# Performance work log

Hardware: AMD Instinct MI355X
Metric: run time of the kernel (lower is better)

## Reference

```python
import jax, jax.numpy as jnp
import numpy as np

# B=batch, T=time, H=hidden_size, D=vocos_dim, I=intermediate_dim, L=num_layers,
# CB=codebook_size, CD=codebook_dim (factorized VQ)
B, T, H, D, I, L, CB, CD = 8, 2048, 1024, 384, 2048, 12, 8192, 8


def _ln(h, g, b, eps=1e-6):
    # torch LayerNorm over last dim (biased variance)
    m = h.mean(-1, keepdims=True)
    v = h.var(-1, keepdims=True)
    return (h - m) / jnp.sqrt(v + eps) * g + b


def _conv1d(x, w, b, groups=1):
    # x: (B, Cin, T), w: (Cout, Cin//groups, 7), same-pad k=7
    y = jax.lax.conv_general_dilated(
        x, w, window_strides=(1,), padding=[(3, 3)],
        dimension_numbers=('NCH', 'OIH', 'NCH'), feature_group_count=groups)
    return y + b[None, :, None]


def setup_inputs() -> dict:
    key = jax.random.key(0)
    ks = iter(jax.random.split(key, 32))
    def nrm(shape):
        return jax.random.normal(next(ks), shape, jnp.float32) * 0.02
    d = {}
    d['x'] = jax.random.normal(next(ks), (B, T, H), jnp.float32)
    # VocosBackbone (encoder): embed conv + LN + 12 ConvNeXt blocks + final LN
    d['enc_embed_w'] = nrm((D, H, 7)); d['enc_embed_b'] = jnp.zeros((D,), jnp.float32)
    d['enc_norm_g'] = jnp.ones((D,), jnp.float32); d['enc_norm_b'] = jnp.zeros((D,), jnp.float32)
    d['enc_dw_w'] = nrm((L, D, 1, 7)); d['enc_dw_b'] = jnp.zeros((L, D), jnp.float32)
    d['enc_ln_g'] = jnp.ones((L, D), jnp.float32); d['enc_ln_b'] = jnp.zeros((L, D), jnp.float32)
    d['enc_w1'] = nrm((L, I, D)); d['enc_b1'] = jnp.zeros((L, I), jnp.float32)
    d['enc_w2'] = nrm((L, D, I)); d['enc_b2'] = jnp.zeros((L, D), jnp.float32)
    d['enc_gamma'] = jnp.full((L, D), 1.0 / L, jnp.float32)  # layer_scale init 1/num_layers
    d['enc_fnorm_g'] = jnp.ones((D,), jnp.float32); d['enc_fnorm_b'] = jnp.zeros((D,), jnp.float32)
    # nn.Linear(vocos_dim, hidden_size)
    d['enc_out_w'] = nrm((H, D)); d['enc_out_b'] = jnp.zeros((H,), jnp.float32)
    # Factorized ResidualVQ (single quantizer): 1024 -> 8, 8192-entry codebook, 8 -> 1024
    d['vq_in_w'] = nrm((CD, H)); d['vq_in_b'] = jnp.zeros((CD,), jnp.float32)
    d['codebook'] = jax.random.normal(next(ks), (CB, CD), jnp.float32)
    d['vq_out_w'] = nrm((H, CD)); d['vq_out_b'] = jnp.zeros((H,), jnp.float32)
    return d


def _encode(x, ew, eb, ng, nb, dww, dwb, lng, lnb, w1, b1, w2, b2, gamma, fg, fb, ow, ob):
    # x: (B, T, H) -> encoder output (B, T, H)
    h = _conv1d(x.transpose(0, 2, 1), ew, eb)            # (B, D, T)
    h = _ln(h.transpose(0, 2, 1), ng, nb)                # (B, T, D)
    for i in range(L):
        res = h
        y = _conv1d(h.transpose(0, 2, 1), dww[i], dwb[i], groups=D)  # depthwise (B, D, T)
        y = _ln(y.transpose(0, 2, 1), lng[i], lnb[i])                # (B, T, D)
        y = jax.nn.gelu(y @ w1[i].T + b1[i], approximate=False)       # (B, T, I)
        y = (y @ w2[i].T + b2[i]) * gamma[i]                          # (B, T, D)
        h = res + y
    h = _ln(h, fg, fb)
    return h @ ow.T + ob                                  # (B, T, H)


def _quantize(enc, in_w, in_b, codebook, out_w, out_b):
    z_e = enc @ in_w.T + in_b                             # (B, T, CD)
    z_n = z_e / jnp.maximum(jnp.linalg.norm(z_e, axis=-1, keepdims=True), 1e-12)
    cb_n = codebook / jnp.maximum(jnp.linalg.norm(codebook, axis=-1, keepdims=True), 1e-12)
    sim = jnp.einsum('btd,nd->btn', z_n, cb_n)            # cosine sim == argmin l2 on normalized vecs
    idx = jnp.argmax(sim, axis=-1)                        # (B, T) int
    z_q = codebook[idx]                                   # (B, T, CD) unnormalized codebook entries
    z_q = z_e + jax.lax.stop_gradient(z_q - z_e)          # straight-through estimator
    quantized = z_q @ out_w.T + out_b                     # (B, T, H)
    return idx, quantized


def reference(x, enc_embed_w, enc_embed_b, enc_norm_g, enc_norm_b, enc_dw_w, enc_dw_b,
              enc_ln_g, enc_ln_b, enc_w1, enc_b1, enc_w2, enc_b2, enc_gamma,
              enc_fnorm_g, enc_fnorm_b, enc_out_w, enc_out_b,
              vq_in_w, vq_in_b, codebook, vq_out_w, vq_out_b):
    enc = _encode(x, enc_embed_w, enc_embed_b, enc_norm_g, enc_norm_b, enc_dw_w, enc_dw_b,
                  enc_ln_g, enc_ln_b, enc_w1, enc_b1, enc_w2, enc_b2, enc_gamma,
                  enc_fnorm_g, enc_fnorm_b, enc_out_w, enc_out_b)
    idx, quantized = _quantize(enc, vq_in_w, vq_in_b, codebook, vq_out_w, vq_out_b)
    # RepCodec.quantize returns (indices (B,T), quantized_out.transpose(1,2) -> (B,T,H))
    return idx, quantized
```

## Files before the change

### kernel.cpp

```cpp
#include <hip/hip_runtime.h>
#include <math.h>


typedef _Float16 h8_t __attribute__((ext_vector_type(8)));
typedef _Float16 h4_t __attribute__((ext_vector_type(4)));
typedef float f4_t __attribute__((ext_vector_type(4)));

__device__ __forceinline__ float gelu_exact(float x){
  return 0.5f * x * (1.0f + erff(x * 0.70710678118654752f));
}

__device__ __forceinline__ void split4(const float4& a, h4_t& hi, h4_t& lo){
  float f[4] = {a.x,a.y,a.z,a.w};
  #pragma unroll
  for (int t=0;t<4;t++){
    _Float16 hh = (_Float16)f[t];
    hi[t] = hh;
    lo[t] = (_Float16)(f[t] - (float)hh);
  }
}

__device__ __forceinline__ int swz(int row, int kg){
  return row*32 + ((kg ^ ((row>>1)&3))<<3);
}

__device__ __forceinline__ void xcd_remap(int& bx, int& by){
  const int gx = gridDim.x;
  const int nwg = gx * gridDim.y;
  int bid = by*gx + bx;
  if ((nwg & 7) == 0){
    bid = (bid & 7)*(nwg >> 3) + (bid >> 3);
    bx = bid % gx; by = bid / gx;
  }
}


__global__ __launch_bounds__(256) void prep_wk_split(const float* __restrict__ w,
                                                     _Float16* __restrict__ wh,
                                                     _Float16* __restrict__ wl){
  int i = blockIdx.x*256 + threadIdx.x;
  if (i >= 384*1024) return;
  int d = i >> 10, c = i & 1023;
  #pragma unroll
  for (int k=0;k<7;k++){
    float v = w[(size_t)d*(1024*7) + (size_t)c*7 + k];
    _Float16 hh = (_Float16)v;
    wh[(size_t)k*393216 + i] = hh;
    wl[(size_t)k*393216 + i] = (_Float16)(v - (float)hh);
  }
}

__global__ __launch_bounds__(256) void prep_cb(const float* __restrict__ cb, float* __restrict__ cbn){
  int e = blockIdx.x*256 + threadIdx.x;
  if (e >= 8192) return;
  float v[8], s = 0.f;
  #pragma unroll
  for (int cd=0; cd<8; ++cd){ v[cd] = cb[(size_t)e*8+cd]; s += v[cd]*v[cd]; }
  float inv = 1.0f / fmaxf(sqrtf(s), 1e-12f);
  #pragma unroll
  for (int cd=0; cd<8; ++cd) cbn[(size_t)e*8+cd] = v[cd]*inv;
}

__global__ __launch_bounds__(256) void split_pair(const float* __restrict__ a, const float* __restrict__ b,
                                                  _Float16* __restrict__ ah, _Float16* __restrict__ al,
                                                  _Float16* __restrict__ bh, _Float16* __restrict__ bl,
                                                  int n4){
  int i = blockIdx.x*256 + threadIdx.x;
  if (i >= n4) return;
  h4_t hi, lo;
  float4 va = ((const float4*)a)[i];
  split4(va, hi, lo);
  ((h4_t*)ah)[i] = hi; ((h4_t*)al)[i] = lo;
  float4 vb = ((const float4*)b)[i];
  split4(vb, hi, lo);
  ((h4_t*)bh)[i] = hi; ((h4_t*)bl)[i] = lo;
}

__global__ __launch_bounds__(256) void split_one(const float* __restrict__ a,
                                                 _Float16* __restrict__ ah, _Float16* __restrict__ al,
                                                 int n4){
  int i = blockIdx.x*256 + threadIdx.x;
  if (i >= n4) return;
  h4_t hi, lo;
  float4 va = ((const float4*)a)[i];
  split4(va, hi, lo);
  ((h4_t*)ah)[i] = hi; ((h4_t*)al)[i] = lo;
}

template<int BN, int EPI>
__global__ __launch_bounds__(256,2) void gemm_s(
    const _Float16* __restrict__ Ah, const _Float16* __restrict__ Al, int lda,
    const _Float16* __restrict__ Bh, const _Float16* __restrict__ Bl, int ldb,
    const float* __restrict__ bias, const float* __restrict__ gamma,
    float* __restrict__ C, _Float16* __restrict__ Ch, _Float16* __restrict__ Cl,
    int ldc, int K)
{
  constexpr int NF = BN/32;
  __shared__ _Float16 AsH[4096], AsL[4096];
  __shared__ _Float16 BsH[BN*32], BsL[BN*32];
  const int tid = threadIdx.x;
  int bx = blockIdx.x, by = blockIdx.y;
  xcd_remap(bx, by);
  const int m0 = by*128, n0 = bx*BN;
  const int srow = tid>>2, kgs = tid&3, koff = kgs*8;
  const _Float16* pAh = Ah + (size_t)(m0+srow)*lda + koff;
  const _Float16* pAl = Al + (size_t)(m0+srow)*lda + koff;
  const _Float16* pBh = Bh + (size_t)(n0+srow)*ldb + koff;
  const _Float16* pBl = Bl + (size_t)(n0+srow)*ldb + koff;
  const int sA0 = swz(srow, kgs), sA1 = swz(srow+64, kgs);
  const int lane = tid & 63, wid = tid >> 6;
  const int wm = (wid>>1)*64, wn = (wid&1)*(BN/2);
  const int fr = lane & 15, kg = lane >> 4;
  f4_t acc[4][NF] = {};
  h8_t rah0 = *(const h8_t*)(pAh);
  h8_t rah1 = *(const h8_t*)(pAh + (size_t)64*lda);
  h8_t ral0 = *(const h8_t*)(pAl);
  h8_t ral1 = *(const h8_t*)(pAl + (size_t)64*lda);
  h8_t rbh0 = *(const h8_t*)(pBh);
  h8_t rbl0 = *(const h8_t*)(pBl);
  h8_t rbh1, rbl1;
  if constexpr (BN == 128){
    rbh1 = *(const h8_t*)(pBh + (size_t)64*ldb);
    rbl1 = *(const h8_t*)(pBl + (size_t)64*ldb);
  }
  for (int k0 = 0; k0 < K; k0 += 32){
    __syncthreads();
    *(h8_t*)(AsH + sA0) = rah0; *(h8_t*)(AsL + sA0) = ral0;
    *(h8_t*)(AsH + sA1) = rah1; *(h8_t*)(AsL + sA1) = ral1;
    *(h8_t*)(BsH + sA0) = rbh0; *(h8_t*)(BsL + sA0) = rbl0;
    if constexpr (BN == 128){
      *(h8_t*)(BsH + sA1) = rbh1; *(h8_t*)(BsL + sA1) = rbl1;
    }
    if (k0 + 32 < K){
      const int kn = k0 + 32;
      rah0 = *(const h8_t*)(pAh + kn);
      rah1 = *(const h8_t*)(pAh + (size_t)64*lda + kn);
      ral0 = *(const h8_t*)(pAl + kn);
      ral1 = *(const h8_t*)(pAl + (size_t)64*lda + kn);
      rbh0 = *(const h8_t*)(pBh + kn);
      rbl0 = *(const h8_t*)(pBl + kn);
      if constexpr (BN == 128){
        rbh1 = *(const h8_t*)(pBh + (size_t)64*ldb + kn);
        rbl1 = *(const h8_t*)(pBl + (size_t)64*ldb + kn);
      }
    }
    __syncthreads();
    h8_t ah[4], al[4], bh[NF], bl[NF];
    #pragma unroll
    for (int m=0;m<4;m++){
      int o = swz(wm + fr + m*16, kg);
      ah[m] = *(const h8_t*)(AsH + o);
      al[m] = *(const h8_t*)(AsL + o);
    }
    #pragma unroll
    for (int n=0;n<NF;n++){
      int o = swz(wn + fr + n*16, kg);
      bh[n] = *(const h8_t*)(BsH + o);
      bl[n] = *(const h8_t*)(BsL + o);
    }
    #pragma unroll
    for (int m=0;m<4;m++)
      #pragma unroll
      for (int n=0;n<NF;n++){
        acc[m][n] = __builtin_amdgcn_mfma_f32_16x16x32_f16(al[m], bh[n], acc[m][n], 0,0,0);
        acc[m][n] = __builtin_amdgcn_mfma_f32_16x16x32_f16(ah[m], bl[n], acc[m][n], 0,0,0);
        acc[m][n] = __builtin_amdgcn_mfma_f32_16x16x32_f16(ah[m], bh[n], acc[m][n], 0,0,0);
      }
  }
  float bj[NF], gj[NF];
  #pragma unroll
  for (int n=0;n<NF;n++){
    int col = n0 + wn + n*16 + fr;
    bj[n] = bias ? bias[col] : 0.0f;
    gj[n] = (EPI==2) ? gamma[col] : 0.0f;
  }
  #pragma unroll
  for (int m=0;m<4;m++){
    #pragma unroll
    for (int r=0;r<4;r++){
      const int row = m0 + wm + m*16 + kg*4 + r;
      #pragma unroll
      for (int n=0;n<NF;n++){
        const int col = n0 + wn + n*16 + fr;
        float v = acc[m][n][r] + bj[n];
        if (EPI==0){
          C[(size_t)row*ldc + col] = v;
        } else if (EPI==1){
          v = gelu_exact(v);
          _Float16 hh = (_Float16)v;
          Ch[(size_t)row*ldc + col] = hh;
          Cl[(size_t)row*ldc + col] = (_Float16)(v - (float)hh);
        } else if (EPI==2){
          C[(size_t)row*ldc + col] += gj[n]*v;
        } else {
          _Float16 hh = (_Float16)v;
          Ch[(size_t)row*ldc + col] = hh;
          Cl[(size_t)row*ldc + col] = (_Float16)(v - (float)hh);
        }
      }
    }
  }
}

template<int EPI>
__global__ __launch_bounds__(512,2) void gemm_t(
    const _Float16* __restrict__ Ah, const _Float16* __restrict__ Al, int lda,
    const _Float16* __restrict__ Bh, const _Float16* __restrict__ Bl, int ldb,
    const float* __restrict__ bias,
    _Float16* __restrict__ Ch, _Float16* __restrict__ Cl,
    int ldc, int K)
{
  __shared__ _Float16 AsH[8192], AsL[8192], BsH[4096], BsL[4096];
  const int tid = threadIdx.x;
  int bx = blockIdx.x, by = blockIdx.y;
  xcd_remap(bx, by);
  const int m0 = by*256, n0 = bx*128;
  const int srow = tid>>2, kgs = tid&3, koff = kgs*8;
  const _Float16* pAh = Ah + (size_t)(m0+srow)*lda + koff;
  const _Float16* pAl = Al + (size_t)(m0+srow)*lda + koff;
  const _Float16* pBh = Bh + (size_t)(n0+srow)*ldb + koff;
  const _Float16* pBl = Bl + (size_t)(n0+srow)*ldb + koff;
  const int sA0 = swz(srow, kgs), sA1 = swz(srow+128, kgs);
  const int lane = tid & 63, wid = tid >> 6;
  const int wm = (wid>>1)*64, wn = (wid&1)*64;
  const int fr = lane & 15, kg = lane >> 4;
  f4_t acc[4][4] = {};
  h8_t rah0 = *(const h8_t*)(pAh);
  h8_t rah1 = *(const h8_t*)(pAh + (size_t)128*lda);
  h8_t ral0 = *(const h8_t*)(pAl);
  h8_t ral1 = *(const h8_t*)(pAl + (size_t)128*lda);
  h8_t rbh0 = *(const h8_t*)(pBh);
  h8_t rbl0 = *(const h8_t*)(pBl);
  for (int k0 = 0; k0 < K; k0 += 32){
    __syncthreads();
    *(h8_t*)(AsH + sA0) = rah0; *(h8_t*)(AsL + sA0) = ral0;
    *(h8_t*)(AsH + sA1) = rah1; *(h8_t*)(AsL + sA1) = ral1;
    *(h8_t*)(BsH + sA0) = rbh0; *(h8_t*)(BsL + sA0) = rbl0;
    if (k0 + 32 < K){
      const int kn = k0 + 32;
      rah0 = *(const h8_t*)(pAh + kn);
      rah1 = *(const h8_t*)(pAh + (size_t)128*lda + kn);
      ral0 = *(const h8_t*)(pAl + kn);
      ral1 = *(const h8_t*)(pAl + (size_t)128*lda + kn);
      rbh0 = *(const h8_t*)(pBh + kn);
      rbl0 = *(const h8_t*)(pBl + kn);
    }
    __syncthreads();
    h8_t ah[4], al[4], bh[4], bl[4];
    #pragma unroll
    for (int m=0;m<4;m++){
      int o = swz(wm + fr + m*16, kg);
      ah[m] = *(const h8_t*)(AsH + o);
      al[m] = *(const h8_t*)(AsL + o);
    }
    #pragma unroll
    for (int n=0;n<4;n++){
      int o = swz(wn + fr + n*16, kg);
      bh[n] = *(const h8_t*)(BsH + o);
      bl[n] = *(const h8_t*)(BsL + o);
    }
    #pragma unroll
    for (int m=0;m<4;m++)
      #pragma unroll
      for (int n=0;n<4;n++){
        acc[m][n] = __builtin_amdgcn_mfma_f32_16x16x32_f16(al[m], bh[n], acc[m][n], 0,0,0);
        acc[m][n] = __builtin_amdgcn_mfma_f32_16x16x32_f16(ah[m], bl[n], acc[m][n], 0,0,0);
        acc[m][n] = __builtin_amdgcn_mfma_f32_16x16x32_f16(ah[m], bh[n], acc[m][n], 0,0,0);
      }
  }
  float bj[4];
  #pragma unroll
  for (int n=0;n<4;n++){
    int col = n0 + wn + n*16 + fr;
    bj[n] = bias ? bias[col] : 0.0f;
  }
  #pragma unroll
  for (int m=0;m<4;m++){
    #pragma unroll
    for (int r=0;r<4;r++){
      const int row = m0 + wm + m*16 + kg*4 + r;
      #pragma unroll
      for (int n=0;n<4;n++){
        const int col = n0 + wn + n*16 + fr;
        float v = acc[m][n][r] + bj[n];
        if (EPI==1) v = gelu_exact(v);
        _Float16 hh = (_Float16)v;
        Ch[(size_t)row*ldc + col] = hh;
        Cl[(size_t)row*ldc + col] = (_Float16)(v - (float)hh);
      }
    }
  }
}

__global__ __launch_bounds__(256,2) void embed_f16(
    const _Float16* __restrict__ xh, const _Float16* __restrict__ xl,
    const _Float16* __restrict__ wkh, const _Float16* __restrict__ wkl,
    const float* __restrict__ bias, float* __restrict__ C)
{
  __shared__ _Float16 AsH[4096], AsL[4096], BsH[2048], BsL[2048];
  const int tid = threadIdx.x;
  int bx = blockIdx.x, by = blockIdx.y;
  xcd_remap(bx, by);
  const int m0 = by*128, n0 = bx*64;
  const int srow = tid>>2, kgs = tid&3, koff = kgs*8;
  const int sA0 = swz(srow, kgs), sA1 = swz(srow+64, kgs);
  const int lane = tid & 63, wid = tid >> 6;
  const int wm = (wid>>1)*64, wn = (wid&1)*32;
  const int fr = lane & 15, kg = lane >> 4;
  const int r0 = m0 + srow, r1 = r0 + 64;
  const int t0 = r0 & 2047, t1 = r1 & 2047;
  f4_t acc[4][2] = {};
  const h8_t zero8 = {0,0,0,0,0,0,0,0};
  h8_t rah0, rah1, ral0, ral1, rbh0, rbl0;
  auto load_tile = [&](int kt, h8_t& a0, h8_t& a1, h8_t& l0, h8_t& l1, h8_t& bh, h8_t& bl){
    const int k = kt >> 5;
    const int k0 = (kt & 31) << 5;
    const bool v0 = (unsigned)(t0 + k - 3) < 2048u;
    const bool v1 = (unsigned)(t1 + k - 3) < 2048u;
    a0 = zero8; a1 = zero8; l0 = zero8; l1 = zero8;
    if (v0){
      const size_t o = (size_t)(r0 + k - 3)*1024 + k0 + koff;
      a0 = *(const h8_t*)(xh + o); l0 = *(const h8_t*)(xl + o);
    }
    if (v1){
      const size_t o = (size_t)(r1 + k - 3)*1024 + k0 + koff;
      a1 = *(const h8_t*)(xh + o); l1 = *(const h8_t*)(xl + o);
    }
    const size_t wo = (size_t)k*393216 + (size_t)(n0+srow)*1024 + k0 + koff;
    bh = *(const h8_t*)(wkh + wo); bl = *(const h8_t*)(wkl + wo);
  };
  load_tile(0, rah0, rah1, ral0, ral1, rbh0, rbl0);
  for (int kt = 0; kt < 224; ++kt){
    __syncthreads();
    *(h8_t*)(AsH+sA0) = rah0; *(h8_t*)(AsL+sA0) = ral0;
    *(h8_t*)(AsH+sA1) = rah1; *(h8_t*)(AsL+sA1) = ral1;
    *(h8_t*)(BsH+sA0) = rbh0; *(h8_t*)(BsL+sA0) = rbl0;
    if (kt + 1 < 224)
      load_tile(kt+1, rah0, rah1, ral0, ral1, rbh0, rbl0);
    __syncthreads();
    h8_t ah[4], al[4], bh[2], bl[2];
    #pragma unroll
    for (int m=0;m<4;m++){
      int o = swz(wm + fr + m*16, kg);
      ah[m] = *(const h8_t*)(AsH + o);
      al[m] = *(const h8_t*)(AsL + o);
    }
    #pragma unroll
    for (int n=0;n<2;n++){
      int o = swz(wn + fr + n*16, kg);
      bh[n] = *(const h8_t*)(BsH + o);
      bl[n] = *(const h8_t*)(BsL + o);
    }
    #pragma unroll
    for (int m=0;m<4;m++)
      #pragma unroll
      for (int n=0;n<2;n++){
        acc[m][n] = __builtin_amdgcn_mfma_f32_16x16x32_f16(al[m], bh[n], acc[m][n], 0,0,0);
        acc[m][n] = __builtin_amdgcn_mfma_f32_16x16x32_f16(ah[m], bl[n], acc[m][n], 0,0,0);
        acc[m][n] = __builtin_amdgcn_mfma_f32_16x16x32_f16(ah[m], bh[n], acc[m][n], 0,0,0);
      }
  }
  #pragma unroll
  for (int m=0;m<4;m++){
    #pragma unroll
    for (int r=0;r<4;r++){
      const int row = m0 + wm + m*16 + kg*4 + r;
      #pragma unroll
      for (int n=0;n<2;n++){
        const int col = n0 + wn + n*16 + fr;
        C[(size_t)row*384 + col] = acc[m][n][r] + bias[col];
      }
    }
  }
}

template<bool CONV, bool SPLIT>
__global__ __launch_bounds__(384) void ln_kernel(
    const float* __restrict__ in,
    const float* __restrict__ dw, const float* __restrict__ db,
    const float* __restrict__ g, const float* __restrict__ b,
    float* __restrict__ out, _Float16* __restrict__ oh, _Float16* __restrict__ ol)
{
  __shared__ float rs[6], rs2[6], stat[2];
  const int m = blockIdx.x, d = threadIdx.x;
  float v;
  if (CONV){
    const int t = m & 2047;
    float a = db[d];
    #pragma unroll
    for (int k=0;k<7;k++){
      int tt = t + k - 3;
      if ((unsigned)tt < 2048u) a = fmaf(in[(size_t)(m + k - 3)*384 + d], dw[d*7 + k], a);
    }
    v = a;
  } else {
    v = in[(size_t)m*384 + d];
  }
  float s = v, s2 = v*v;
  #pragma unroll
  for (int o=1;o<64;o<<=1){ s += __shfl_xor(s,o); s2 += __shfl_xor(s2,o); }
  const int wid = d >> 6, lane = d & 63;
  if (lane == 0){ rs[wid]=s; rs2[wid]=s2; }
  __syncthreads();
  if (d == 0){
    float S=0.f, S2=0.f;
    #pragma unroll
    for (int w=0;w<6;w++){ S+=rs[w]; S2+=rs2[w]; }
    float mean = S*(1.0f/384.0f);
    float var = fmaxf(S2*(1.0f/384.0f) - mean*mean, 0.0f);
    stat[0]=mean; stat[1]=1.0f/sqrtf(var + 1e-6f);
  }
  __syncthreads();
  float o = (v - stat[0])*stat[1]*g[d] + b[d];
  if (SPLIT){
    _Float16 hh = (_Float16)o;
    oh[(size_t)m*384 + d] = hh;
    ol[(size_t)m*384 + d] = (_Float16)(o - (float)hh);
  } else {
    out[(size_t)m*384 + d] = o;
  }
}


__global__ __launch_bounds__(256) void vq_in_kernel(
    const _Float16* __restrict__ ench, const _Float16* __restrict__ encl,
    const float* __restrict__ wi, const float* __restrict__ bi, float* __restrict__ zn)
{
  __shared__ float sw[8192];
  const int tid = threadIdx.x;
  for (int i = tid*4; i < 8192; i += 1024) *(float4*)&sw[i] = *(const float4*)&wi[i];
  __syncthreads();
  const int wid = tid >> 6, lane = tid & 63;
  const size_t m = (size_t)blockIdx.x*4 + wid;
  float acc[8] = {};
  for (int j=0;j<16;j++){
    float v = (float)ench[m*1024 + j*64 + lane] + (float)encl[m*1024 + j*64 + lane];
    #pragma unroll
    for (int cd=0;cd<8;cd++) acc[cd] = fmaf(v, sw[cd*1024 + j*64 + lane], acc[cd]);
  }
  #pragma unroll
  for (int cd=0;cd<8;cd++)
    #pragma unroll
    for (int o=1;o<64;o<<=1) acc[cd] += __shfl_xor(acc[cd], o);
  if (lane == 0){
    float z[8], s = 0.f;
    #pragma unroll
    for (int cd=0;cd<8;cd++){ z[cd] = acc[cd] + bi[cd]; s += z[cd]*z[cd]; }
    float inv = 1.0f / fmaxf(sqrtf(s), 1e-12f);
    #pragma unroll
    for (int cd=0;cd<8;cd++) zn[m*8+cd] = z[cd]*inv;
  }
}

__global__ __launch_bounds__(256) void vq_argmax(
    const float* __restrict__ zn, const float* __restrict__ cbn,
    int* __restrict__ idx_out, float* __restrict__ idx_f)
{
  __shared__ float sbest[256];
  __shared__ int   sidx[256];
  const int tid = threadIdx.x;
  const int tok = tid & 31, ch = tid >> 5;
  const size_t m = (size_t)blockIdx.x*32 + tok;
  float4 z0 = *(const float4*)&zn[m*8];
  float4 z1 = *(const float4*)&zn[m*8+4];
  float best = -1e30f; int bidx = 0;
  const float* cp = cbn + (size_t)ch*8192;
  #pragma unroll 4
  for (int e = 0; e < 1024; ++e){
    const float4 ca  = *(const float4*)&cp[e*8];
    const float4 cb4 = *(const float4*)&cp[e*8+4];
    float s = z0.x*ca.x + z0.y*ca.y + z0.z*ca.z + z0.w*ca.w
            + z1.x*cb4.x + z1.y*cb4.y + z1.z*cb4.z + z1.w*cb4.w;
    if (s > best){ best = s; bidx = ch*1024 + e; }
  }
  sbest[tid] = best; sidx[tid] = bidx;
  __syncthreads();
  if (tid < 32){
    float b = sbest[tid]; int bi = sidx[tid];
    #pragma unroll
    for (int c=1;c<8;c++){
      float ob = sbest[c*32 + tid];
      if (ob > b){ b = ob; bi = sidx[c*32 + tid]; }
    }
    idx_out[(size_t)blockIdx.x*32 + tid] = bi;
    idx_f [(size_t)blockIdx.x*32 + tid] = (float)bi;
  }
}

__global__ __launch_bounds__(256) void vq_out_kernel(
    const int* __restrict__ idx, const float* __restrict__ cb,
    const float* __restrict__ wo, const float* __restrict__ bo,
    float* __restrict__ outq)
{
  __shared__ float wT[8][1024];
  __shared__ float cbs[16][8];
  __shared__ int idxs[16];
  const int tid = threadIdx.x;
  #pragma unroll
  for (int j=0;j<4;j++){
    int hcol = j*256 + tid;
    float4 w0 = *(const float4*)&wo[(size_t)hcol*8];
    float4 w1 = *(const float4*)&wo[(size_t)hcol*8+4];
    wT[0][hcol]=w0.x; wT[1][hcol]=w0.y; wT[2][hcol]=w0.z; wT[3][hcol]=w0.w;
    wT[4][hcol]=w1.x; wT[5][hcol]=w1.y; wT[6][hcol]=w1.z; wT[7][hcol]=w1.w;
  }
  if (tid < 16) idxs[tid] = idx[blockIdx.x*16 + tid];
  __syncthreads();
  if (tid < 128){ int tk = tid>>3, cd = tid&7; cbs[tk][cd] = cb[(size_t)idxs[tk]*8 + cd]; }
  __syncthreads();
  float bb[4];
  #pragma unroll
  for (int j=0;j<4;j++) bb[j] = bo[j*256+tid];
  for (int tk=0;tk<16;tk++){
    const size_t m = (size_t)blockIdx.x*16 + tk;
    float c0=cbs[tk][0], c1=cbs[tk][1], c2=cbs[tk][2], c3=cbs[tk][3];
    float c4=cbs[tk][4], c5=cbs[tk][5], c6=cbs[tk][6], c7=cbs[tk][7];
    #pragma unroll
    for (int j=0;j<4;j++){
      int hcol = j*256 + tid;
      float v = bb[j];
      v = fmaf(c0, wT[0][hcol], v); v = fmaf(c1, wT[1][hcol], v);
      v = fmaf(c2, wT[2][hcol], v); v = fmaf(c3, wT[3][hcol], v);
      v = fmaf(c4, wT[4][hcol], v); v = fmaf(c5, wT[5][hcol], v);
      v = fmaf(c6, wT[6][hcol], v); v = fmaf(c7, wT[7][hcol], v);
      outq[m*1024 + hcol] = v;
    }
  }
}


extern "C" void kernel_launch(void* const* d_in, const int* in_sizes, int n_in,
                              void* d_out, int out_size, void* d_ws, size_t ws_size,
                              hipStream_t stream) {
  (void)in_sizes; (void)n_in; (void)out_size; (void)ws_size;
  const float* x   = (const float*)d_in[0];
  const float* eww = (const float*)d_in[1];
  const float* ewb = (const float*)d_in[2];
  const float* ng  = (const float*)d_in[3];
  const float* nb  = (const float*)d_in[4];
  const float* dww = (const float*)d_in[5];
  const float* dwb = (const float*)d_in[6];
  const float* lng = (const float*)d_in[7];
  const float* lnb = (const float*)d_in[8];
  const float* w1  = (const float*)d_in[9];
  const float* b1  = (const float*)d_in[10];
  const float* w2  = (const float*)d_in[11];
  const float* b2  = (const float*)d_in[12];
  const float* gma = (const float*)d_in[13];
  const float* fg  = (const float*)d_in[14];
  const float* fb  = (const float*)d_in[15];
  const float* ow  = (const float*)d_in[16];
  const float* ob  = (const float*)d_in[17];
  const float* viw = (const float*)d_in[18];
  const float* vib = (const float*)d_in[19];
  const float* cb  = (const float*)d_in[20];
  const float* vow = (const float*)d_in[21];
  const float* vob = (const float*)d_in[22];
  float* out = (float*)d_out;

  float* ws = (float*)d_ws;
  float* wreg = ws;
  _Float16* wkh = (_Float16*)wreg;
  _Float16* wkl = wkh + 2752512;
  _Float16* w1h = (_Float16*)wreg;
  _Float16* w1l = w1h + 786432;
  _Float16* w2h = w1h + 1572864;
  _Float16* w2l = w1h + 2359296;
  _Float16* owh = (_Float16*)wreg;
  _Float16* owl = owh + 393216;
  float* zn  = wreg + 1048576;
  float* cbn = wreg + 1179648;
  int*  idxb = (int*)(wreg + 1245184);
  float* h   = ws + 2752512;
  float* ylreg = ws + 9043968;
  float* yf32 = ylreg;
  _Float16* ylh = (_Float16*)ylreg;
  _Float16* yll = ylh + 6291456;
  float* y1reg = ws + 15335424;
  _Float16* xh  = (_Float16*)y1reg;
  _Float16* xl  = xh + 16777216;
  _Float16* y1h = (_Float16*)y1reg;
  _Float16* y1l = y1h + 16777216;
  _Float16* ench = y1h;
  _Float16* encl = y1l;

  prep_wk_split<<<dim3(1536), dim3(256), 0, stream>>>(eww, wkh, wkl);
  split_one<<<dim3(16384), dim3(256), 0, stream>>>(x, xh, xl, 4194304);
  embed_f16<<<dim3(6,128), dim3(256), 0, stream>>>(xh, xl, wkh, wkl, ewb, yf32);
  ln_kernel<false,false><<<dim3(16384), dim3(384), 0, stream>>>(
      yf32, nullptr, nullptr, ng, nb, h, nullptr, nullptr);

  for (int i = 0; i < 12; ++i){
    split_pair<<<dim3(768), dim3(256), 0, stream>>>(
        w1 + (size_t)i*786432, w2 + (size_t)i*786432, w1h, w1l, w2h, w2l, 196608);
    ln_kernel<true,true><<<dim3(16384), dim3(384), 0, stream>>>(
        h, dww + (size_t)i*2688, dwb + (size_t)i*384,
        lng + (size_t)i*384, lnb + (size_t)i*384, nullptr, ylh, yll);
    for (int ic = 0; ic < 2; ++ic){
      gemm_t<1><<<dim3(8,64), dim3(512), 0, stream>>>(
          ylh, yll, 384,
          w1h + (size_t)ic*393216, w1l + (size_t)ic*393216, 384,
          b1 + (size_t)i*2048 + (size_t)ic*1024,
          y1h, y1l, 1024, 384);
      gemm_s<64,2><<<dim3(6,128), dim3(256), 0, stream>>>(
          y1h, y1l, 1024,
          w2h + (size_t)ic*1024, w2l + (size_t)ic*1024, 2048,
          (ic == 0) ? (b2 + (size_t)i*384) : nullptr,
          gma + (size_t)i*384,
          h, nullptr, nullptr, 384, 1024);
    }
  }

  ln_kernel<false,true><<<dim3(16384), dim3(384), 0, stream>>>(
      h, nullptr, nullptr, fg, fb, nullptr, ylh, yll);
  split_one<<<dim3(384), dim3(256), 0, stream>>>(ow, owh, owl, 98304);
  gemm_t<3><<<dim3(8,64), dim3(512), 0, stream>>>(
      ylh, yll, 384, owh, owl, 384, ob, ench, encl, 1024, 384);

  prep_cb<<<dim3(32), dim3(256), 0, stream>>>(cb, cbn);
  vq_in_kernel<<<dim3(4096), dim3(256), 0, stream>>>(ench, encl, viw, vib, zn);
  vq_argmax<<<dim3(512), dim3(256), 0, stream>>>(zn, cbn, idxb, out);
  vq_out_kernel<<<dim3(1024), dim3(256), 0, stream>>>(idxb, cb, vow, vob, out + 16384);
}
```

Measured before the change: 3.732 ms.

## Fold enc_out and vq_in projections, retile GEMMs with K=64 stages and setprio

Precomputes vq_in_w @ enc_out_w (8x384) and the matching combined bias, so the 1024-wide encoder output GEMM and its fp16 split are dropped and z_e is computed straight from the final LayerNorm output. The first FFN GEMM moves from gemm_t (256x128 tiles, 512 threads) to gemm_s<128> with 256 threads. The second FFN GEMM and the embed conv become a new gemm64-style kernel that stages 64-wide K tiles. MFMA blocks are wrapped in s_setprio. Folding the two linear maps changes the float rounding order, which could flip argmax ties, and the larger LDS tiles may lower occupancy.

```diff
diff --git a/kernel.cpp b/kernel.cpp
--- a/kernel.cpp
+++ b/kernel.cpp
@@ -59,6 +59,25 @@
   float inv = 1.0f / fmaxf(sqrtf(s), 1e-12f);
   #pragma unroll
   for (int cd=0; cd<8; ++cd) cbn[(size_t)e*8+cd] = v[cd]*inv;
+}
+
+__global__ __launch_bounds__(256) void prep_cw(const float* __restrict__ viw, const float* __restrict__ ow,
+                                               const float* __restrict__ vib, const float* __restrict__ ob,
+                                               float* __restrict__ cw, float* __restrict__ cbias){
+  int i = blockIdx.x*256 + threadIdx.x;
+  if (i < 3072){
+    int c = i / 384, d = i - c*384;
+    float acc = 0.f;
+    for (int h=0; h<1024; ++h)
+      acc = fmaf(viw[c*1024+h], ow[(size_t)h*384 + d], acc);
+    cw[i] = acc;
+  }
+  if (blockIdx.x == 0 && threadIdx.x < 8){
+    int c = threadIdx.x;
+    float acc = vib[c];
+    for (int h=0; h<1024; ++h) acc = fmaf(viw[c*1024+h], ob[h], acc);
+    cbias[c] = acc;
+  }
 }
 
 __global__ __launch_bounds__(256) void split_pair(const float* __restrict__ a, const float* __restrict__ b,
@@ -91,8 +110,8 @@
 __global__ __launch_bounds__(256,2) void gemm_s(
     const _Float16* __restrict__ Ah, const _Float16* __restrict__ Al, int lda,
     const _Float16* __restrict__ Bh, const _Float16* __restrict__ Bl, int ldb,
-    const float* __restrict__ bias, const float* __restrict__ gamma,
-    float* __restrict__ C, _Float16* __restrict__ Ch, _Float16* __restrict__ Cl,
+    const float* __restrict__ bias,
+    _Float16* __restrict__ Ch, _Float16* __restrict__ Cl,
     int ldc, int K)
 {
   constexpr int NF = BN/32;
@@ -158,6 +177,7 @@
       bh[n] = *(const h8_t*)(BsH + o);
       bl[n] = *(const h8_t*)(BsL + o);
     }
+    __builtin_amdgcn_s_setprio(1);
     #pragma unroll
     for (int m=0;m<4;m++)
       #pragma unroll
@@ -166,14 +186,11 @@
         acc[m][n] = __builtin_amdgcn_mfma_f32_16x16x32_f16(ah[m], bl[n], acc[m][n], 0,0,0);
         acc[m][n] = __builtin_amdgcn_mfma_f32_16x16x32_f16(ah[m], bh[n], acc[m][n], 0,0,0);
       }
-  }
-  float bj[NF], gj[NF];
-  #pragma unroll
-  for (int n=0;n<NF;n++){
-    int col = n0 + wn + n*16 + fr;
-    bj[n] = bias ? bias[col] : 0.0f;
-    gj[n] = (EPI==2) ? gamma[col] : 0.0f;
-  }
+    __builtin_amdgcn_s_setprio(0);
+  }
+  float bj[NF];
+  #pragma unroll
+  for (int n=0;n<NF;n++) bj[n] = bias ? bias[n0 + wn + n*16 + fr] : 0.0f;
   #pragma unroll
   for (int m=0;m<4;m++){
     #pragma unroll
@@ -181,106 +198,6 @@
       const int row = m0 + wm + m*16 + kg*4 + r;
       #pragma unroll
       for (int n=0;n<NF;n++){
-        const int col = n0 + wn + n*16 + fr;
-        float v = acc[m][n][r] + bj[n];
-        if (EPI==0){
-          C[(size_t)row*ldc + col] = v;
-        } else if (EPI==1){
-          v = gelu_exact(v);
-          _Float16 hh = (_Float16)v;
-          Ch[(size_t)row*ldc + col] = hh;
-          Cl[(size_t)row*ldc + col] = (_Float16)(v - (float)hh);
-        } else if (EPI==2){
-          C[(size_t)row*ldc + col] += gj[n]*v;
-        } else {
-          _Float16 hh = (_Float16)v;
-          Ch[(size_t)row*ldc + col] = hh;
-          Cl[(size_t)row*ldc + col] = (_Float16)(v - (float)hh);
-        }
-      }
-    }
-  }
-}
-
-template<int EPI>
-__global__ __launch_bounds__(512,2) void gemm_t(
-    const _Float16* __restrict__ Ah, const _Float16* __restrict__ Al, int lda,
-    const _Float16* __restrict__ Bh, const _Float16* __restrict__ Bl, int ldb,
-    const float* __restrict__ bias,
-    _Float16* __restrict__ Ch, _Float16* __restrict__ Cl,
-    int ldc, int K)
-{
-  __shared__ _Float16 AsH[8192], AsL[8192], BsH[4096], BsL[4096];
-  const int tid = threadIdx.x;
-  int bx = blockIdx.x, by = blockIdx.y;
-  xcd_remap(bx, by);
-  const int m0 = by*256, n0 = bx*128;
-  const int srow = tid>>2, kgs = tid&3, koff = kgs*8;
-  const _Float16* pAh = Ah + (size_t)(m0+srow)*lda + koff;
-  const _Float16* pAl = Al + (size_t)(m0+srow)*lda + koff;
-  const _Float16* pBh = Bh + (size_t)(n0+srow)*ldb + koff;
-  const _Float16* pBl = Bl + (size_t)(n0+srow)*ldb + koff;
-  const int sA0 = swz(srow, kgs), sA1 = swz(srow+128, kgs);
-  const int lane = tid & 63, wid = tid >> 6;
-  const int wm = (wid>>1)*64, wn = (wid&1)*64;
-  const int fr = lane & 15, kg = lane >> 4;
-  f4_t acc[4][4] = {};
-  h8_t rah0 = *(const h8_t*)(pAh);
-  h8_t rah1 = *(const h8_t*)(pAh + (size_t)128*lda);
-  h8_t ral0 = *(const h8_t*)(pAl);
-  h8_t ral1 = *(const h8_t*)(pAl + (size_t)128*lda);
-  h8_t rbh0 = *(const h8_t*)(pBh);
-  h8_t rbl0 = *(const h8_t*)(pBl);
-  for (int k0 = 0; k0 < K; k0 += 32){
-    __syncthreads();
-    *(h8_t*)(AsH + sA0) = rah0; *(h8_t*)(AsL + sA0) = ral0;
-    *(h8_t*)(AsH + sA1) = rah1; *(h8_t*)(AsL + sA1) = ral1;
-    *(h8_t*)(BsH + sA0) = rbh0; *(h8_t*)(BsL + sA0) = rbl0;
-    if (k0 + 32 < K){
-      const int kn = k0 + 32;
-      rah0 = *(const h8_t*)(pAh + kn);
-      rah1 = *(const h8_t*)(pAh + (size_t)128*lda + kn);
-      ral0 = *(const h8_t*)(pAl + kn);
-      ral1 = *(const h8_t*)(pAl + (size_t)128*lda + kn);
-      rbh0 = *(const h8_t*)(pBh + kn);
-      rbl0 = *(const h8_t*)(pBl + kn);
-    }
-    __syncthreads();
-    h8_t ah[4], al[4], bh[4], bl[4];
-    #pragma unroll
-    for (int m=0;m<4;m++){
-      int o = swz(wm + fr + m*16, kg);
-      ah[m] = *(const h8_t*)(AsH + o);
-      al[m] = *(const h8_t*)(AsL + o);
-    }
-    #pragma unroll
-    for (int n=0;n<4;n++){
-      int o = swz(wn + fr + n*16, kg);
-      bh[n] = *(const h8_t*)(BsH + o);
-      bl[n] = *(const h8_t*)(BsL + o);
-    }
-    #pragma unroll
-    for (int m=0;m<4;m++)
-      #pragma unroll
-      for (int n=0;n<4;n++){
-        acc[m][n] = __builtin_amdgcn_mfma_f32_16x16x32_f16(al[m], bh[n], acc[m][n], 0,0,0);
-        acc[m][n] = __builtin_amdgcn_mfma_f32_16x16x32_f16(ah[m], bl[n], acc[m][n], 0,0,0);
-        acc[m][n] = __builtin_amdgcn_mfma_f32_16x16x32_f16(ah[m], bh[n], acc[m][n], 0,0,0);
-      }
-  }
-  float bj[4];
-  #pragma unroll
-  for (int n=0;n<4;n++){
-    int col = n0 + wn + n*16 + fr;
-    bj[n] = bias ? bias[col] : 0.0f;
-  }
-  #pragma unroll
-  for (int m=0;m<4;m++){
-    #pragma unroll
-    for (int r=0;r<4;r++){
-      const int row = m0 + wm + m*16 + kg*4 + r;
-      #pragma unroll
-      for (int n=0;n<4;n++){
         const int col = n0 + wn + n*16 + fr;
         float v = acc[m][n][r] + bj[n];
         if (EPI==1) v = gelu_exact(v);
@@ -292,73 +209,188 @@
   }
 }
 
+__global__ __launch_bounds__(256,2) void gemm64(
+    const _Float16* __restrict__ Ah, const _Float16* __restrict__ Al, int lda,
+    const _Float16* __restrict__ Bh, const _Float16* __restrict__ Bl, int ldb,
+    const float* __restrict__ bias, const float* __restrict__ gamma,
+    float* __restrict__ C, int ldc, int K)
+{
+  __shared__ _Float16 AsH[8192], AsL[8192];
+  __shared__ _Float16 BsH[4096], BsL[4096];
+  const int tid = threadIdx.x;
+  int bx = blockIdx.x, by = blockIdx.y;
+  xcd_remap(bx, by);
+  const int m0 = by*128, n0 = bx*64;
+  const int srowA = tid>>1, khA = tid&1;
+  const int srowB = tid>>2, kgB = tid&3;
+  const _Float16* pAh = Ah + (size_t)(m0+srowA)*lda + khA*32;
+  const _Float16* pAl = Al + (size_t)(m0+srowA)*lda + khA*32;
+  const _Float16* pBh = Bh + (size_t)(n0+srowB)*ldb + kgB*8;
+  const _Float16* pBl = Bl + (size_t)(n0+srowB)*ldb + kgB*8;
+  const int lane = tid & 63, wid = tid >> 6;
+  const int wm = (wid>>1)*64, wn = (wid&1)*32;
+  const int fr = lane & 15, kg = lane >> 4;
+  f4_t acc[4][2] = {};
+  h8_t rAh[4], rAl[4], rBh[2], rBl[2];
+  auto gload = [&](int k0){
+    #pragma unroll
+    for (int j=0;j<4;j++){
+      rAh[j] = *(const h8_t*)(pAh + k0 + j*8);
+      rAl[j] = *(const h8_t*)(pAl + k0 + j*8);
+    }
+    #pragma unroll
+    for (int t=0;t<2;t++){
+      rBh[t] = *(const h8_t*)(pBh + k0 + t*32);
+      rBl[t] = *(const h8_t*)(pBl + k0 + t*32);
+    }
+  };
+  gload(0);
+  const int nt = K >> 6;
+  for (int it = 0; it < nt; ++it){
+    __syncthreads();
+    #pragma unroll
+    for (int j=0;j<4;j++){
+      int slot = khA*4096 + swz(srowA, j);
+      *(h8_t*)(AsH + slot) = rAh[j];
+      *(h8_t*)(AsL + slot) = rAl[j];
+    }
+    #pragma unroll
+    for (int t=0;t<2;t++){
+      int slot = t*2048 + swz(srowB, kgB);
+      *(h8_t*)(BsH + slot) = rBh[t];
+      *(h8_t*)(BsL + slot) = rBl[t];
+    }
+    if (it + 1 < nt) gload((it+1) << 6);
+    __syncthreads();
+    #pragma unroll
+    for (int s=0;s<2;s++){
+      h8_t ah[4], al[4], bh[2], bl[2];
+      #pragma unroll
+      for (int m=0;m<4;m++){
+        int o = s*4096 + swz(wm + fr + m*16, kg);
+        ah[m] = *(const h8_t*)(AsH + o);
+        al[m] = *(const h8_t*)(AsL + o);
+      }
+      #pragma unroll
+      for (int n=0;n<2;n++){
+        int o = s*2048 + swz(wn + fr + n*16, kg);
+        bh[n] = *(const h8_t*)(BsH + o);
+        bl[n] = *(const h8_t*)(BsL + o);
+      }
+      __builtin_amdgcn_s_setprio(1);
+      #pragma unroll
+      for (int m=0;m<4;m++)
+        #pragma unroll
+        for (int n=0;n<2;n++){
+          acc[m][n] = __builtin_amdgcn_mfma_f32_16x16x32_f16(al[m], bh[n], acc[m][n], 0,0,0);
+          acc[m][n] = __builtin_amdgcn_mfma_f32_16x16x32_f16(ah[m], bl[n], acc[m][n], 0,0,0);
+          acc[m][n] = __builtin_amdgcn_mfma_f32_16x16x32_f16(ah[m], bh[n], acc[m][n], 0,0,0);
+        }
+      __builtin_amdgcn_s_setprio(0);
+    }
+  }
+  float bj[2], gj[2];
+  #pragma unroll
+  for (int n=0;n<2;n++){
+    int col = n0 + wn + n*16 + fr;
+    bj[n] = bias ? bias[col] : 0.0f;
+    gj[n] = gamma[col];
+  }
+  #pragma unroll
+  for (int m=0;m<4;m++){
+    #pragma unroll
+    for (int r=0;r<4;r++){
+      const int row = m0 + wm + m*16 + kg*4 + r;
+      #pragma unroll
+      for (int n=0;n<2;n++){
+        const int col = n0 + wn + n*16 + fr;
+        C[(size_t)row*ldc + col] += gj[n]*(acc[m][n][r] + bj[n]);
+      }
+    }
+  }
+}
+
 __global__ __launch_bounds__(256,2) void embed_f16(
     const _Float16* __restrict__ xh, const _Float16* __restrict__ xl,
     const _Float16* __restrict__ wkh, const _Float16* __restrict__ wkl,
     const float* __restrict__ bias, float* __restrict__ C)
 {
-  __shared__ _Float16 AsH[4096], AsL[4096], BsH[2048], BsL[2048];
+  __shared__ _Float16 AsH[8192], AsL[8192], BsH[4096], BsL[4096];
   const int tid = threadIdx.x;
   int bx = blockIdx.x, by = blockIdx.y;
   xcd_remap(bx, by);
   const int m0 = by*128, n0 = bx*64;
-  const int srow = tid>>2, kgs = tid&3, koff = kgs*8;
-  const int sA0 = swz(srow, kgs), sA1 = swz(srow+64, kgs);
+  const int srowA = tid>>1, khA = tid&1;
+  const int srowB = tid>>2, kgB = tid&3;
+  const int rA = m0 + srowA, tA = rA & 2047;
   const int lane = tid & 63, wid = tid >> 6;
   const int wm = (wid>>1)*64, wn = (wid&1)*32;
   const int fr = lane & 15, kg = lane >> 4;
-  const int r0 = m0 + srow, r1 = r0 + 64;
-  const int t0 = r0 & 2047, t1 = r1 & 2047;
   f4_t acc[4][2] = {};
   const h8_t zero8 = {0,0,0,0,0,0,0,0};
-  h8_t rah0, rah1, ral0, ral1, rbh0, rbl0;
-  auto load_tile = [&](int kt, h8_t& a0, h8_t& a1, h8_t& l0, h8_t& l1, h8_t& bh, h8_t& bl){
-    const int k = kt >> 5;
-    const int k0 = (kt & 31) << 5;
-    const bool v0 = (unsigned)(t0 + k - 3) < 2048u;
-    const bool v1 = (unsigned)(t1 + k - 3) < 2048u;
-    a0 = zero8; a1 = zero8; l0 = zero8; l1 = zero8;
-    if (v0){
-      const size_t o = (size_t)(r0 + k - 3)*1024 + k0 + koff;
-      a0 = *(const h8_t*)(xh + o); l0 = *(const h8_t*)(xl + o);
-    }
-    if (v1){
-      const size_t o = (size_t)(r1 + k - 3)*1024 + k0 + koff;
-      a1 = *(const h8_t*)(xh + o); l1 = *(const h8_t*)(xl + o);
-    }
-    const size_t wo = (size_t)k*393216 + (size_t)(n0+srow)*1024 + k0 + koff;
-    bh = *(const h8_t*)(wkh + wo); bl = *(const h8_t*)(wkl + wo);
+  h8_t rAh[4], rAl[4], rBh[2], rBl[2];
+  auto load_tile = [&](int it){
+    const int k = it >> 4;
+    const int k0 = (it & 15) << 6;
+    const bool v = (unsigned)(tA + k - 3) < 2048u;
+    const _Float16* ph = xh + (size_t)(rA + k - 3)*1024 + k0 + khA*32;
+    const _Float16* pl = xl + (size_t)(rA + k - 3)*1024 + k0 + khA*32;
+    #pragma unroll
+    for (int j=0;j<4;j++){
+      rAh[j] = v ? *(const h8_t*)(ph + j*8) : zero8;
+      rAl[j] = v ? *(const h8_t*)(pl + j*8) : zero8;
+    }
+    const _Float16* qh = wkh + (size_t)k*393216 + (size_t)(n0+srowB)*1024 + k0 + kgB*8;
+    const _Float16* ql = wkl + (size_t)k*393216 + (size_t)(n0+srowB)*1024 + k0 + kgB*8;
+    #pragma unroll
+    for (int t=0;t<2;t++){
+      rBh[t] = *(const h8_t*)(qh + t*32);
+      rBl[t] = *(const h8_t*)(ql + t*32);
+    }
   };
-  load_tile(0, rah0, rah1, ral0, ral1, rbh0, rbl0);
-  for (int kt = 0; kt < 224; ++kt){
+  load_tile(0);
+  for (int it = 0; it < 112; ++it){
     __syncthreads();
-    *(h8_t*)(AsH+sA0) = rah0; *(h8_t*)(AsL+sA0) = ral0;
-    *(h8_t*)(AsH+sA1) = rah1; *(h8_t*)(AsL+sA1) = ral1;
-    *(h8_t*)(BsH+sA0) = rbh0; *(h8_t*)(BsL+sA0) = rbl0;
-    if (kt + 1 < 224)
-      load_tile(kt+1, rah0, rah1, ral0, ral1, rbh0, rbl0);
+    #pragma unroll
+    for (int j=0;j<4;j++){
+      int slot = khA*4096 + swz(srowA, j);
+      *(h8_t*)(AsH + slot) = rAh[j];
+      *(h8_t*)(AsL + slot) = rAl[j];
+    }
+    #pragma unroll
+    for (int t=0;t<2;t++){
+      int slot = t*2048 + swz(srowB, kgB);
+      *(h8_t*)(BsH + slot) = rBh[t];
+      *(h8_t*)(BsL + slot) = rBl[t];
+    }
+    if (it + 1 < 112) load_tile(it + 1);
     __syncthreads();
-    h8_t ah[4], al[4], bh[2], bl[2];
-    #pragma unroll
-    for (int m=0;m<4;m++){
-      int o = swz(wm + fr + m*16, kg);
-      ah[m] = *(const h8_t*)(AsH + o);
-      al[m] = *(const h8_t*)(AsL + o);
-    }
-    #pragma unroll
-    for (int n=0;n<2;n++){
-      int o = swz(wn + fr + n*16, kg);
-      bh[n] = *(const h8_t*)(BsH + o);
-      bl[n] = *(const h8_t*)(BsL + o);
-    }
-    #pragma unroll
-    for (int m=0;m<4;m++)
+    #pragma unroll
+    for (int s=0;s<2;s++){
+      h8_t ah[4], al[4], bh[2], bl[2];
+      #pragma unroll
+      for (int m=0;m<4;m++){
+        int o = s*4096 + swz(wm + fr + m*16, kg);
+        ah[m] = *(const h8_t*)(AsH + o);
+        al[m] = *(const h8_t*)(AsL + o);
+      }
       #pragma unroll
       for (int n=0;n<2;n++){
-        acc[m][n] = __builtin_amdgcn_mfma_f32_16x16x32_f16(al[m], bh[n], acc[m][n], 0,0,0);
-        acc[m][n] = __builtin_amdgcn_mfma_f32_16x16x32_f16(ah[m], bl[n], acc[m][n], 0,0,0);
-        acc[m][n] = __builtin_amdgcn_mfma_f32_16x16x32_f16(ah[m], bh[n], acc[m][n], 0,0,0);
-      }
+        int o = s*2048 + swz(wn + fr + n*16, kg);
+        bh[n] = *(const h8_t*)(BsH + o);
+        bl[n] = *(const h8_t*)(BsL + o);
+      }
+      __builtin_amdgcn_s_setprio(1);
+      #pragma unroll
+      for (int m=0;m<4;m++)
+        #pragma unroll
+        for (int n=0;n<2;n++){
+          acc[m][n] = __builtin_amdgcn_mfma_f32_16x16x32_f16(al[m], bh[n], acc[m][n], 0,0,0);
+          acc[m][n] = __builtin_amdgcn_mfma_f32_16x16x32_f16(ah[m], bl[n], acc[m][n], 0,0,0);
+          acc[m][n] = __builtin_amdgcn_mfma_f32_16x16x32_f16(ah[m], bh[n], acc[m][n], 0,0,0);
+        }
+      __builtin_amdgcn_s_setprio(0);
+    }
   }
   #pragma unroll
   for (int m=0;m<4;m++){
@@ -422,21 +454,22 @@
 }
 
 
-__global__ __launch_bounds__(256) void vq_in_kernel(
-    const _Float16* __restrict__ ench, const _Float16* __restrict__ encl,
-    const float* __restrict__ wi, const float* __restrict__ bi, float* __restrict__ zn)
+__global__ __launch_bounds__(256) void vq_ze(
+    const float* __restrict__ y, const float* __restrict__ cw,
+    const float* __restrict__ cbias, float* __restrict__ zn)
 {
-  __shared__ float sw[8192];
+  __shared__ float scw[3072];
   const int tid = threadIdx.x;
-  for (int i = tid*4; i < 8192; i += 1024) *(float4*)&sw[i] = *(const float4*)&wi[i];
+  for (int i = tid; i < 3072; i += 256) scw[i] = cw[i];
   __syncthreads();
   const int wid = tid >> 6, lane = tid & 63;
   const size_t m = (size_t)blockIdx.x*4 + wid;
   float acc[8] = {};
-  for (int j=0;j<16;j++){
-    float v = (float)ench[m*1024 + j*64 + lane] + (float)encl[m*1024 + j*64 + lane];
-    #pragma unroll
-    for (int cd=0;cd<8;cd++) acc[cd] = fmaf(v, sw[cd*1024 + j*64 + lane], acc[cd]);
+  #pragma unroll
+  for (int j=0;j<6;j++){
+    float v = y[m*384 + j*64 + lane];
+    #pragma unroll
+    for (int cd=0;cd<8;cd++) acc[cd] = fmaf(v, scw[cd*384 + j*64 + lane], acc[cd]);
   }
   #pragma unroll
   for (int cd=0;cd<8;cd++)
@@ -445,7 +478,7 @@
   if (lane == 0){
     float z[8], s = 0.f;
     #pragma unroll
-    for (int cd=0;cd<8;cd++){ z[cd] = acc[cd] + bi[cd]; s += z[cd]*z[cd]; }
+    for (int cd=0;cd<8;cd++){ z[cd] = acc[cd] + cbias[cd]; s += z[cd]*z[cd]; }
     float inv = 1.0f / fmaxf(sqrtf(s), 1e-12f);
     #pragma unroll
     for (int cd=0;cd<8;cd++) zn[m*8+cd] = z[cd]*inv;
@@ -566,11 +599,11 @@
   _Float16* w1l = w1h + 786432;
   _Float16* w2h = w1h + 1572864;
   _Float16* w2l = w1h + 2359296;
-  _Float16* owh = (_Float16*)wreg;
-  _Float16* owl = owh + 393216;
   float* zn  = wreg + 1048576;
   float* cbn = wreg + 1179648;
   int*  idxb = (int*)(wreg + 1245184);
+  float* cw  = wreg + 1261568;
+  float* cbias = wreg + 1264640;
   float* h   = ws + 2752512;
   float* ylreg = ws + 9043968;
   float* yf32 = ylreg;
@@ -581,8 +614,6 @@
   _Float16* xl  = xh + 16777216;
   _Float16* y1h = (_Float16*)y1reg;
   _Float16* y1l = y1h + 16777216;
-  _Float16* ench = y1h;
-  _Float16* encl = y1l;
 
   prep_wk_split<<<dim3(1536), dim3(256), 0, stream>>>(eww, wkh, wkl);
   split_one<<<dim3(16384), dim3(256), 0, stream>>>(x, xh, xl, 4194304);
@@ -597,28 +628,25 @@
         h, dww + (size_t)i*2688, dwb + (size_t)i*384,
         lng + (size_t)i*384, lnb + (size_t)i*384, nullptr, ylh, yll);
     for (int ic = 0; ic < 2; ++ic){
-      gemm_t<1><<<dim3(8,64), dim3(512), 0, stream>>>(
+      gemm_s<128,1><<<dim3(8,128), dim3(256), 0, stream>>>(
           ylh, yll, 384,
           w1h + (size_t)ic*393216, w1l + (size_t)ic*393216, 384,
           b1 + (size_t)i*2048 + (size_t)ic*1024,
           y1h, y1l, 1024, 384);
-      gemm_s<64,2><<<dim3(6,128), dim3(256), 0, stream>>>(
+      gemm64<<<dim3(6,128), dim3(256), 0, stream>>>(
           y1h, y1l, 1024,
           w2h + (size_t)ic*1024, w2l + (size_t)ic*1024, 2048,
           (ic == 0) ? (b2 + (size_t)i*384) : nullptr,
           gma + (size_t)i*384,
-          h, nullptr, nullptr, 384, 1024);
-    }
-  }
-
-  ln_kernel<false,true><<<dim3(16384), dim3(384), 0, stream>>>(
-      h, nullptr, nullptr, fg, fb, nullptr, ylh, yll);
-  split_one<<<dim3(384), dim3(256), 0, stream>>>(ow, owh, owl, 98304);
-  gemm_t<3><<<dim3(8,64), dim3(512), 0, stream>>>(
-      ylh, yll, 384, owh, owl, 384, ob, ench, encl, 1024, 384);
-
+          h, 384, 1024);
+    }
+  }
+
+  ln_kernel<false,false><<<dim3(16384), dim3(384), 0, stream>>>(
+      h, nullptr, nullptr, fg, fb, yf32, nullptr, nullptr);
+  prep_cw<<<dim3(12), dim3(256), 0, stream>>>(viw, ow, vib, ob, cw, cbias);
   prep_cb<<<dim3(32), dim3(256), 0, stream>>>(cb, cbn);
-  vq_in_kernel<<<dim3(4096), dim3(256), 0, stream>>>(ench, encl, viw, vib, zn);
+  vq_ze<<<dim3(4096), dim3(256), 0, stream>>>(yf32, cw, cbias, zn);
   vq_argmax<<<dim3(512), dim3(256), 0, stream>>>(zn, cbn, idxb, out);
   vq_out_kernel<<<dim3(1024), dim3(256), 0, stream>>>(idxb, cb, vow, vob, out + 16384);
 }
```

Measured after the change: 3.761 ms. About the same (+0.8%).
